# Kernel tuning notes

Hardware: AMD Instinct MI355X
Metric: run time of the kernel (lower is better)

The kernel has to match this reference:

```python
import jax, jax.numpy as jnp
import numpy as np

P, C, D = 65536, 64, 256

def setup_inputs() -> dict:
    key = jax.random.key(0)
    k1, k2, k3, k4 = jax.random.split(key, 4)
    return {
        "protos1": jax.random.normal(k1, (P, D), dtype=jnp.float32),
        "protos2": jax.random.normal(k2, (P, D), dtype=jnp.float32),
        "W": jax.random.normal(k3, (D, D), dtype=jnp.float32) / np.float32(np.sqrt(D)),
        "b": jax.random.normal(k4, (D,), dtype=jnp.float32),
        "num_classes": C,
    }

def _pairwise_dist(x, y):
    # x: (C, n, D), y: (C, m, D) -> squared-euclidean-style dists (C, n, m)
    xs = jnp.sum(x * x, axis=-1)[:, :, None]
    ys = jnp.sum(y * y, axis=-1)[:, None, :]
    return xs + ys - 2.0 * jnp.einsum('cid,cjd->cij', x, y)

def reference(protos1, protos2, W, b, num_classes):
    nc = int(num_classes)
    d = protos1.shape[-1]
    # prototypes[c::num_classes] for all c at once: (P,D) -> (P//C, C, D) -> (C, P//C, D)
    p1 = protos1.reshape(-1, nc, d).transpose(1, 0, 2)
    p2 = protos2.reshape(-1, nc, d).transpose(1, 0, 2)
    # transition: nn.Linear -> x @ W.T + b ; inverse: (x - b) @ inv(W.T)
    p2_inv = (p2 - b) @ jnp.linalg.inv(W.T)
    p1_fwd = p1 @ W.T + b
    a = _pairwise_dist(p1, p2_inv)          # (C, n, n)
    bb = _pairwise_dist(p2, p1_fwd)         # (C, n, n)
    proto_losses_source = jnp.mean(jnp.min(a, axis=2), axis=1)   # (C,)
    proto_losses_target = jnp.mean(jnp.min(bb, axis=2), axis=1)  # (C,)
    return jnp.stack([proto_losses_source, proto_losses_target])  # (2, C)
```

## Files before the change

kernel.cpp:

```cpp
#include <hip/hip_runtime.h>

#define D 256
#define NC 64

using u16 = unsigned short;
using u32 = unsigned int;

typedef __attribute__((ext_vector_type(8))) short bfv8;
typedef __attribute__((ext_vector_type(4))) float f32x4;

__device__ __forceinline__ float bf2f(u32 u) {
  union { u32 i; float f; } v; v.i = u << 16; return v.f;
}
__device__ __forceinline__ u16 f2bf(float f) {
  union { float f; u32 i; } v; v.f = f;
  u32 x = v.i;
  return (u16)((x + 0x7FFFu + ((x >> 16) & 1u)) >> 16);
}
__device__ __forceinline__ u32 pk2(float a, float b) {
  return (u32)f2bf(a) | ((u32)f2bf(b) << 16);
}
__device__ __forceinline__ size_t cmrow(int g) {
  return (size_t)(((g & 63) << 10) | (g >> 6));
}

__device__ __forceinline__ void gload_lds16(const void* src, void* dst) {
  __builtin_amdgcn_global_load_lds(
      (const __attribute__((address_space(1))) void*)src,
      (__attribute__((address_space(3))) void*)dst, 16, 0, 0);
}

#define PH_LDS 70912
#define DIST_LDS 66560

__device__ void gj_body(const float* __restrict__ W, float* __restrict__ IW,
                        char* smem) {
  float (*Ml)[20]    = (float(*)[20])smem;
  float (*Arow)[256] = (float(*)[256])(smem + 20480);
  float (*G)[256]    = (float(*)[256])(smem + 36864);
  u16*  Gfrag        = (u16*)(smem + 53248);
  float (*Pinv)[20]  = (float(*)[20])(smem + 69632);
  const int t = threadIdx.x, w = t >> 6, l = t & 63;
  const int lj = l & 15, lh = l >> 4;
  const int r0 = 16 * w;

  f32x4 x[16];
#pragma unroll
  for (int ct = 0; ct < 16; ++ct)
#pragma unroll
    for (int reg = 0; reg < 4; ++reg)
      x[ct][reg] = W[(size_t)(r0 + 4 * lh + reg) * D + 16 * ct + lj];

  for (int s = 0; s < 16; ++s) {
#pragma unroll
    for (int ct = 0; ct < 16; ++ct)
      if (ct == s)
#pragma unroll
        for (int reg = 0; reg < 4; ++reg)
          Ml[r0 + 4 * lh + reg][lj] = x[ct][reg];
    if (w == s) {
#pragma unroll
      for (int ct = 0; ct < 16; ++ct)
#pragma unroll
        for (int reg = 0; reg < 4; ++reg)
          Arow[4 * lh + reg][16 * ct + lj] = x[ct][reg];
    }
    __syncthreads();
    if (t < 16) {
      float p[16];
      {
        float4 rr0 = *(const float4*)&Ml[16 * s + t][0];
        float4 rr1 = *(const float4*)&Ml[16 * s + t][4];
        float4 rr2 = *(const float4*)&Ml[16 * s + t][8];
        float4 rr3 = *(const float4*)&Ml[16 * s + t][12];
        p[0] = rr0.x; p[1] = rr0.y; p[2] = rr0.z; p[3] = rr0.w;
        p[4] = rr1.x; p[5] = rr1.y; p[6] = rr1.z; p[7] = rr1.w;
        p[8] = rr2.x; p[9] = rr2.y; p[10] = rr2.z; p[11] = rr2.w;
        p[12] = rr3.x; p[13] = rr3.y; p[14] = rr3.z; p[15] = rr3.w;
      }
#pragma unroll
      for (int pp = 0; pp < 16; ++pp) {
        float u[16];
#pragma unroll
        for (int j = 0; j < 16; ++j)
          u[j] = __int_as_float(__builtin_amdgcn_readlane(__float_as_int(p[j]), pp));
        const float pv = u[pp];
        const float d = 1.0f / pv;
        if (t == pp) {
#pragma unroll
          for (int j = 0; j < 16; ++j) p[j] = u[j] * d;
          p[pp] = d;
        } else {
          const float md = p[pp] * d;
          u[pp] = pv + 1.0f;
#pragma unroll
          for (int j = 0; j < 16; ++j) p[j] = fmaf(-md, u[j], p[j]);
        }
      }
#pragma unroll
      for (int j = 0; j < 16; ++j) Pinv[t][j] = p[j];
    }
    __syncthreads();
    {
      const bool inC = ((l >> 2) == s);
      const int co = (l & 3) << 2;
      const int gct = l >> 2;
      const int kk = w;
      float4 g = make_float4(0.f, 0.f, 0.f, 0.f);
#pragma unroll
      for (int q = 0; q < 16; ++q) {
        const float pv = Pinv[kk][q];
        const float4 av = *(const float4*)&Arow[q][4 * l];
        g.x = fmaf(pv, av.x, g.x); g.y = fmaf(pv, av.y, g.y);
        g.z = fmaf(pv, av.z, g.z); g.w = fmaf(pv, av.w, g.w);
      }
      if (inC) {
        g.x = Pinv[kk][co + 0] + (kk == co + 0 ? 1.f : 0.f);
        g.y = Pinv[kk][co + 1] + (kk == co + 1 ? 1.f : 0.f);
        g.z = Pinv[kk][co + 2] + (kk == co + 2 ? 1.f : 0.f);
        g.w = Pinv[kk][co + 3] + (kk == co + 3 ? 1.f : 0.f);
      }
      *(float4*)&G[kk][4 * l] = g;
      const int e0 = kk & 7;
      const int lbase = 16 * (kk >> 3);
      const float gv[4] = {g.x, g.y, g.z, g.w};
#pragma unroll
      for (int cc = 0; cc < 4; ++cc) {
        const int cl = 4 * (l & 3) + cc;
        const u16 hi = f2bf(gv[cc]);
        const u16 lo = f2bf(gv[cc] - bf2f(hi));
        Gfrag[(gct * 64 + lbase + cl) * 8 + e0] = hi;
        Gfrag[(gct * 64 + 32 + lbase + cl) * 8 + e0] = lo;
      }
    }
    __syncthreads();
    bfv8 afr;
    {
      const int row = r0 + lj;
      float4 f0 = *(const float4*)&Ml[row][8 * (lh & 1)];
      float4 f1 = *(const float4*)&Ml[row][8 * (lh & 1) + 4];
      const float fv[8] = {f0.x, f0.y, f0.z, f0.w, f1.x, f1.y, f1.z, f1.w};
      union { bfv8 v; u16 e[8]; } A;
      if (lh < 2) {
#pragma unroll
        for (int e = 0; e < 8; ++e) A.e[e] = f2bf(-fv[e]);
      } else {
#pragma unroll
        for (int e = 0; e < 8; ++e) {
          const float hi = bf2f(f2bf(fv[e]));
          A.e[e] = f2bf(-(fv[e] - hi));
        }
      }
      afr = A.v;
    }
    if (w != s) {
#pragma unroll
      for (int ct = 0; ct < 16; ++ct) {
        bfv8 b1 = *(const bfv8*)&Gfrag[(ct * 64 + l) * 8];
        bfv8 b2 = *(const bfv8*)&Gfrag[(ct * 64 + (l ^ 32)) * 8];
        x[ct] = __builtin_amdgcn_mfma_f32_16x16x32_bf16(afr, b1, x[ct], 0, 0, 0);
        x[ct] = __builtin_amdgcn_mfma_f32_16x16x32_bf16(afr, b2, x[ct], 0, 0, 0);
      }
    } else {
#pragma unroll
      for (int ct = 0; ct < 16; ++ct) {
        if (ct == s) {
#pragma unroll
          for (int reg = 0; reg < 4; ++reg)
            x[ct][reg] = Pinv[4 * lh + reg][lj];
        } else {
#pragma unroll
          for (int reg = 0; reg < 4; ++reg)
            x[ct][reg] = G[4 * lh + reg][16 * ct + lj];
        }
      }
    }
    __syncthreads();
  }
#pragma unroll
  for (int ct = 0; ct < 16; ++ct)
#pragma unroll
    for (int reg = 0; reg < 4; ++reg)
      IW[(size_t)(r0 + 4 * lh + reg) * D + 16 * ct + lj] = x[ct][reg];
}

template <int MODE, bool WRITE_NRM>
__device__ void prep_body(const float* __restrict__ Ain,
                          const u16* __restrict__ Brows,
                          const float* __restrict__ biasv,
                          u16* __restrict__ Out, float* __restrict__ nrm,
                          float* __restrict__ nfp, int it, char* smem) {
  const int tx = threadIdx.x, ww = tx >> 6, l = tx & 63;
  const int mw = ww >> 3, nw = ww & 7, l4 = l >> 4, lm = l & 15;
  char* Ab = smem;
  float* nfpart = (float*)(smem + 65536);

  bfv8 bfr[2][8];
#pragma unroll
  for (int nf2 = 0; nf2 < 2; ++nf2)
#pragma unroll
    for (int ks = 0; ks < 8; ++ks)
      bfr[nf2][ks] = *(const bfv8*)(Brows +
          (size_t)(nw * 32 + nf2 * 16 + lm) * D + ks * 32 + l4 * 8);

  {
    const int r = tx >> 3, sg = tx & 7;
    const float* arow = Ain + (size_t)(it * 128 + r) * D + sg * 32;
    float ss = 0.f;
#pragma unroll
    for (int g2 = 0; g2 < 4; ++g2) {
      float4 v0 = *(const float4*)(arow + g2 * 8);
      float4 v1 = *(const float4*)(arow + g2 * 8 + 4);
      ss = fmaf(v0.x, v0.x, fmaf(v0.y, v0.y, fmaf(v0.z, v0.z, fmaf(v0.w, v0.w, ss))));
      ss = fmaf(v1.x, v1.x, fmaf(v1.y, v1.y, fmaf(v1.z, v1.z, fmaf(v1.w, v1.w, ss))));
      uint4 w4;
      w4.x = pk2(v0.x, v0.y); w4.y = pk2(v0.z, v0.w);
      w4.z = pk2(v1.x, v1.y); w4.w = pk2(v1.z, v1.w);
      *(uint4*)(Ab + (sg * 8 + (r >> 4)) * 1024 + ((r & 15) + g2 * 16) * 16) = w4;
    }
    ss += __shfl_xor(ss, 1, 64);
    ss += __shfl_xor(ss, 2, 64);
    ss += __shfl_xor(ss, 4, 64);
    if (WRITE_NRM && sg == 0) nrm[cmrow(it * 128 + r)] = ss;
  }
  __syncthreads();

  const bfv8* A8 = (const bfv8*)Ab;
  f32x4 acc[4][2];
#pragma unroll
  for (int mf = 0; mf < 4; ++mf) {
    acc[mf][0] = f32x4{0.f, 0.f, 0.f, 0.f};
    acc[mf][1] = f32x4{0.f, 0.f, 0.f, 0.f};
  }
#pragma unroll
  for (int ks = 0; ks < 8; ++ks)
#pragma unroll
    for (int mf = 0; mf < 4; ++mf) {
      bfv8 a = A8[(ks * 8 + mw * 4 + mf) * 64 + l];
      acc[mf][0] = __builtin_amdgcn_mfma_f32_16x16x32_bf16(a, bfr[0][ks], acc[mf][0], 0, 0, 0);
      acc[mf][1] = __builtin_amdgcn_mfma_f32_16x16x32_bf16(a, bfr[1][ks], acc[mf][1], 0, 0, 0);
    }

  float bias[2];
  if (MODE == 0) {
#pragma unroll
    for (int nf2 = 0; nf2 < 2; ++nf2)
      bias[nf2] = biasv[nw * 32 + nf2 * 16 + lm];
  } else {
#pragma unroll
    for (int nf2 = 0; nf2 < 2; ++nf2) {
      float pd = 0.f;
#pragma unroll
      for (int ks = 0; ks < 8; ++ks) {
        float4 b0 = *(const float4*)(biasv + ks * 32 + l4 * 8);
        float4 b1 = *(const float4*)(biasv + ks * 32 + l4 * 8 + 4);
        pd = fmaf(b0.x, bf2f((u16)bfr[nf2][ks][0]), pd);
        pd = fmaf(b0.y, bf2f((u16)bfr[nf2][ks][1]), pd);
        pd = fmaf(b0.z, bf2f((u16)bfr[nf2][ks][2]), pd);
        pd = fmaf(b0.w, bf2f((u16)bfr[nf2][ks][3]), pd);
        pd = fmaf(b1.x, bf2f((u16)bfr[nf2][ks][4]), pd);
        pd = fmaf(b1.y, bf2f((u16)bfr[nf2][ks][5]), pd);
        pd = fmaf(b1.z, bf2f((u16)bfr[nf2][ks][6]), pd);
        pd = fmaf(b1.w, bf2f((u16)bfr[nf2][ks][7]), pd);
      }
      pd += __shfl_xor(pd, 16, 64);
      pd += __shfl_xor(pd, 32, 64);
      bias[nf2] = -pd;
    }
  }

#pragma unroll
  for (int mf = 0; mf < 4; ++mf)
#pragma unroll
    for (int rr = 0; rr < 4; ++rr) {
      const int g = it * 128 + mw * 64 + mf * 16 + l4 * 4 + rr;
      const size_t orow = cmrow(g) * D;
      float v2 = 0.f;
#pragma unroll
      for (int nf2 = 0; nf2 < 2; ++nf2) {
        const float v = acc[mf][nf2][rr] + bias[nf2];
        const u16 hv = f2bf(v);
        Out[orow + nw * 32 + nf2 * 16 + lm] = hv;
        const float vr = bf2f(hv);
        v2 = fmaf(vr, vr, v2);
      }
      v2 += __shfl_xor(v2, 1, 64);
      v2 += __shfl_xor(v2, 2, 64);
      v2 += __shfl_xor(v2, 4, 64);
      v2 += __shfl_xor(v2, 8, 64);
      if (lm == 0) nfpart[nw * 128 + mw * 64 + mf * 16 + l4 * 4 + rr] = v2;
    }
  __syncthreads();
  if (tx < 128) {
    float s = 0.f;
#pragma unroll
    for (int q = 0; q < 8; ++q) s += nfpart[q * 128 + tx];
    nfp[cmrow(it * 128 + tx)] = s;
  }
}

__device__ void norms_role(const float* __restrict__ p2, float* __restrict__ n2,
                           int idx) {
  const int tx = threadIdx.x, q = tx & 3;
#pragma unroll
  for (int rep = 0; rep < 8; ++rep) {
    const int g = idx * 2048 + rep * 256 + (tx >> 2);
    const float* row = p2 + (size_t)g * D + q * 64;
    float ss = 0.f;
#pragma unroll
    for (int g2 = 0; g2 < 16; ++g2) {
      float4 v = *(const float4*)(row + g2 * 4);
      ss = fmaf(v.x, v.x, fmaf(v.y, v.y, fmaf(v.z, v.z, fmaf(v.w, v.w, ss))));
    }
    ss += __shfl_xor(ss, 1, 64);
    ss += __shfl_xor(ss, 2, 64);
    if (q == 0) n2[cmrow(g)] = ss;
  }
}

__global__ __launch_bounds__(1024, 1) void phase1_kernel(
    const float* __restrict__ p1, const float* __restrict__ p2,
    const float* __restrict__ W, const u16* __restrict__ Wb,
    const float* __restrict__ bv, u16* __restrict__ Fb,
    float* __restrict__ n1, float* __restrict__ n2,
    float* __restrict__ nf, float* __restrict__ IWa) {
  extern __shared__ char smem[];
  const int b = blockIdx.x;
  if (b == 0) {
    gj_body(W, IWa, smem);
  } else if (b <= 512) {
    prep_body<0, true>(p1, Wb, bv, Fb, n1, nf, b - 1, smem);
  } else {
    norms_role(p2, n2, b - 513);
  }
}

__global__ __launch_bounds__(1024, 1) void phase3_kernel(
    const float* __restrict__ p2, const u16* __restrict__ IWb,
    const float* __restrict__ bv, u16* __restrict__ Qb,
    float* __restrict__ nq) {
  extern __shared__ char smem[];
  prep_body<1, false>(p2, IWb, bv, Qb, nullptr, nq, blockIdx.x, smem);
}

__global__ __launch_bounds__(256) void nr_residual(const float* __restrict__ W,
                                                   const float* __restrict__ X,
                                                   float* __restrict__ R) {
  __shared__ float wrow[D];
  const int i = blockIdx.x, j = threadIdx.x;
  wrow[j] = W[i * D + j];
  __syncthreads();
  float acc = 0.f;
#pragma unroll 8
  for (int k = 0; k < D; ++k) acc = fmaf(wrow[k], X[k * D + j], acc);
  R[i * D + j] = (i == j ? 2.0f : 0.0f) - acc;
}

__global__ __launch_bounds__(256) void nr_mult_bf16(const float* __restrict__ X,
                                                    const float* __restrict__ R,
                                                    u16* __restrict__ Yb) {
  __shared__ float xrow[D];
  const int i = blockIdx.x, j = threadIdx.x;
  xrow[j] = X[i * D + j];
  __syncthreads();
  float acc = 0.f;
#pragma unroll 8
  for (int k = 0; k < D; ++k) acc = fmaf(xrow[k], R[k * D + j], acc);
  Yb[i * D + j] = f2bf(acc);
}

__global__ __launch_bounds__(256) void wconv(const float* __restrict__ W,
                                             u16* __restrict__ Wb) {
  const int i = blockIdx.x * 256 + threadIdx.x;
  Wb[i] = f2bf(W[i]);
}

__global__ __launch_bounds__(256, 2) void dist_kernel(
    const float* __restrict__ p1, const float* __restrict__ p2,
    const u16* __restrict__ Qb, const u16* __restrict__ Fb,
    const float* __restrict__ n1, const float* __restrict__ n2,
    const float* __restrict__ nq, const float* __restrict__ nf,
    float* __restrict__ partial) {
  extern __shared__ char smem[];
  const int bid = blockIdx.x;
  const int lb = (bid & 7) * 128 + (bid >> 3);
  const int c = lb >> 4, dir = (lb >> 3) & 1, it = lb & 7;
  const float* Ain = dir ? p2 : p1;
  const u16* Bin = dir ? Fb : Qb;
  const float* nA = dir ? n2 : n1;
  const float* nB = dir ? nf : nq;
  const int tx = threadIdx.x, wid = tx >> 6, l = tx & 63;
  const int l4 = l >> 4, lm = l & 15;

  auto issue_b = [&](int half, int jt) {
    const size_t base = ((size_t)(c << 10) + jt * 128) * D;
#pragma unroll
    for (int jf = 0; jf < 8; ++jf) {
      const u16* src = Bin + base + (size_t)(jf * 16 + lm) * D
                       + half * 128 + wid * 32 + l4 * 8;
      gload_lds16(src, smem + half * 32768 + (wid * 8 + jf) * 1024);
    }
  };

  issue_b(0, 0);
  bfv8 afr[2][8];
  const float* abase = Ain + ((size_t)(it * 128 + wid * 32) * NC + c) * D;
#pragma unroll
  for (int m = 0; m < 2; ++m)
#pragma unroll
    for (int ks = 0; ks < 8; ++ks) {
      const float* ap = abase + (size_t)(m * 16 + lm) * (NC * D) + ks * 32 + l4 * 8;
      float4 v0 = *(const float4*)(ap);
      float4 v1 = *(const float4*)(ap + 4);
      union { bfv8 v; uint4 u; } cv;
      cv.u.x = pk2(v0.x, v0.y); cv.u.y = pk2(v0.z, v0.w);
      cv.u.z = pk2(v1.x, v1.y); cv.u.w = pk2(v1.z, v1.w);
      afr[m][ks] = cv.v;
    }
  float na[2][4];
#pragma unroll
  for (int m = 0; m < 2; ++m)
#pragma unroll
    for (int rr = 0; rr < 4; ++rr)
      na[m][rr] = nA[(c << 10) + it * 128 + wid * 32 + m * 16 + l4 * 4 + rr];
  float minv[2][4];
#pragma unroll
  for (int m = 0; m < 2; ++m)
#pragma unroll
    for (int rr = 0; rr < 4; ++rr) minv[m][rr] = 3.0e38f;
  __syncthreads();

  const bfv8* lds8 = (const bfv8*)smem;
  for (int jt = 0; jt < 8; ++jt) {
    f32x4 acc[2][8];
#pragma unroll
    for (int m = 0; m < 2; ++m)
#pragma unroll
      for (int n = 0; n < 8; ++n) acc[m][n] = f32x4{0.f, 0.f, 0.f, 0.f};
    float nbv[8];
#pragma unroll
    for (int n = 0; n < 8; ++n)
      nbv[n] = nB[(c << 10) + jt * 128 + n * 16 + lm];
    issue_b(1, jt);
#pragma unroll
    for (int ks = 0; ks < 4; ++ks) {
      bfv8 bb[8];
#pragma unroll
      for (int n = 0; n < 8; ++n) bb[n] = lds8[(ks * 8 + n) * 64 + l];
#pragma unroll
      for (int m = 0; m < 2; ++m)
#pragma unroll
        for (int n = 0; n < 8; ++n)
          acc[m][n] = __builtin_amdgcn_mfma_f32_16x16x32_bf16(afr[m][ks], bb[n], acc[m][n], 0, 0, 0);
    }
    __syncthreads();
    if (jt < 7) issue_b(0, jt + 1);
#pragma unroll
    for (int ks = 4; ks < 8; ++ks) {
      bfv8 bb[8];
#pragma unroll
      for (int n = 0; n < 8; ++n) bb[n] = lds8[2048 + ((ks - 4) * 8 + n) * 64 + l];
#pragma unroll
      for (int m = 0; m < 2; ++m)
#pragma unroll
        for (int n = 0; n < 8; ++n)
          acc[m][n] = __builtin_amdgcn_mfma_f32_16x16x32_bf16(afr[m][ks], bb[n], acc[m][n], 0, 0, 0);
    }
#pragma unroll
    for (int m = 0; m < 2; ++m)
#pragma unroll
      for (int n = 0; n < 8; ++n)
#pragma unroll
        for (int rr = 0; rr < 4; ++rr) {
          const float dd = na[m][rr] + nbv[n] - 2.0f * acc[m][n][rr];
          minv[m][rr] = fminf(minv[m][rr], dd);
        }
    __syncthreads();
  }
  float* red = (float*)(smem + 65536);
#pragma unroll
  for (int m = 0; m < 2; ++m)
#pragma unroll
    for (int rr = 0; rr < 4; ++rr) {
      float mm = minv[m][rr];
      mm = fminf(mm, __shfl_xor(mm, 1, 64));
      mm = fminf(mm, __shfl_xor(mm, 2, 64));
      mm = fminf(mm, __shfl_xor(mm, 4, 64));
      mm = fminf(mm, __shfl_xor(mm, 8, 64));
      if (lm == 0) red[wid * 32 + m * 16 + l4 * 4 + rr] = mm;
    }
  __syncthreads();
  if (tx < 128) {
    float v = red[tx];
#pragma unroll
    for (int off = 32; off; off >>= 1) v += __shfl_xor(v, off, 64);
    if ((tx & 63) == 0) red[128 + (tx >> 6)] = v;
  }
  __syncthreads();
  if (tx == 0) partial[lb] = red[128] + red[129];
}

__global__ void finalize_kernel(const float* __restrict__ partial,
                                float* __restrict__ out) {
  const int tx = threadIdx.x;
  if (tx >= 128) return;
  const int dir = tx >> 6, c = tx & 63;
  float s = 0.f;
#pragma unroll
  for (int it = 0; it < 8; ++it) s += partial[(c << 4) | (dir << 3) | it];
  out[dir * 64 + c] = s * (1.0f / 1024.0f);
}

extern "C" void kernel_launch(void* const* d_in, const int* in_sizes, int n_in,
                              void* d_out, int out_size, void* d_ws, size_t ws_size,
                              hipStream_t stream) {
  const float* p1 = (const float*)d_in[0];
  const float* p2 = (const float*)d_in[1];
  const float* W  = (const float*)d_in[2];
  const float* bv = (const float*)d_in[3];
  float* out = (float*)d_out;
  char* ws = (char*)d_ws;
  float* n1   = (float*)(ws);
  float* n2   = (float*)(ws + (256 << 10));
  float* nf   = (float*)(ws + (512 << 10));
  float* nq   = (float*)(ws + (768 << 10));
  float* partial = (float*)(ws + (1024 << 10));
  u16* Wb  = (u16*)(ws + (1032 << 10));
  u16* IWb = (u16*)(ws + (1160 << 10));
  float* IWa = (float*)(ws + (1288 << 10));
  float* Rt  = (float*)(ws + (1544 << 10));
  u16* Fb  = (u16*)(ws + (2048 << 10));
  u16* Qb  = (u16*)(ws + (2048 << 10) + (32u << 20));

  hipFuncSetAttribute((const void*)phase1_kernel,
                      hipFuncAttributeMaxDynamicSharedMemorySize, PH_LDS);
  hipFuncSetAttribute((const void*)phase3_kernel,
                      hipFuncAttributeMaxDynamicSharedMemorySize, PH_LDS);
  hipFuncSetAttribute((const void*)dist_kernel,
                      hipFuncAttributeMaxDynamicSharedMemorySize, DIST_LDS);

  wconv<<<256, 256, 0, stream>>>(W, Wb);
  phase1_kernel<<<545, 1024, PH_LDS, stream>>>(p1, p2, W, Wb, bv, Fb,
                                               n1, n2, nf, IWa);
  nr_residual<<<256, 256, 0, stream>>>(W, IWa, Rt);
  nr_mult_bf16<<<256, 256, 0, stream>>>(IWa, Rt, IWb);
  phase3_kernel<<<512, 1024, PH_LDS, stream>>>(p2, IWb, bv, Qb, nq);
  dist_kernel<<<1024, 256, DIST_LDS, stream>>>(p1, p2, Qb, Fb, n1, n2,
                                               nq, nf, partial);
  finalize_kernel<<<1, 128, 0, stream>>>(partial, out);
}
```

Measured before the change: 298.1 us.

## Overlap target-direction distance pass with NR residual and trim Gauss-Jordan syncs

Splits the distance kernel into two directions. The target direction, which needs only the forward projection, now runs alongside the Newton-Schulz residual in a combined kernel before the inverse path finishes. The source direction runs after phase3. Separately, the Gauss-Jordan inverse now has every wave invert the 16x16 pivot block redundantly and broadcast it via readlane, removing one block barrier per step and one at the end of each step. This adds redundant ALU work per wave and a heterogeneous launch with mismatched block roles.

```diff
diff --git a/kernel.cpp b/kernel.cpp
--- a/kernel.cpp
+++ b/kernel.cpp
@@ -35,11 +35,11 @@
 
 __device__ void gj_body(const float* __restrict__ W, float* __restrict__ IW,
                         char* smem) {
-  float (*Ml)[20]    = (float(*)[20])smem;
-  float (*Arow)[256] = (float(*)[256])(smem + 20480);
-  float (*G)[256]    = (float(*)[256])(smem + 36864);
-  u16*  Gfrag        = (u16*)(smem + 53248);
-  float (*Pinv)[20]  = (float(*)[20])(smem + 69632);
+  float (*Arow)[260]   = (float(*)[260])smem;
+  float (*G)[256]      = (float(*)[256])(smem + 16640);
+  u16*  Gfrag          = (u16*)(smem + 33024);
+  float (*Ml)[16][20]  = (float(*)[16][20])(smem + 49408);
+  float (*PinvL)[16]   = (float(*)[16])(smem + 69888);
   const int t = threadIdx.x, w = t >> 6, l = t & 63;
   const int lj = l & 15, lh = l >> 4;
   const int r0 = 16 * w;
@@ -57,7 +57,7 @@
       if (ct == s)
 #pragma unroll
         for (int reg = 0; reg < 4; ++reg)
-          Ml[r0 + 4 * lh + reg][lj] = x[ct][reg];
+          Ml[w][4 * lh + reg][lj] = x[ct][reg];
     if (w == s) {
 #pragma unroll
       for (int ct = 0; ct < 16; ++ct)
@@ -66,18 +66,19 @@
           Arow[4 * lh + reg][16 * ct + lj] = x[ct][reg];
     }
     __syncthreads();
-    if (t < 16) {
-      float p[16];
-      {
-        float4 rr0 = *(const float4*)&Ml[16 * s + t][0];
-        float4 rr1 = *(const float4*)&Ml[16 * s + t][4];
-        float4 rr2 = *(const float4*)&Ml[16 * s + t][8];
-        float4 rr3 = *(const float4*)&Ml[16 * s + t][12];
-        p[0] = rr0.x; p[1] = rr0.y; p[2] = rr0.z; p[3] = rr0.w;
-        p[4] = rr1.x; p[5] = rr1.y; p[6] = rr1.z; p[7] = rr1.w;
-        p[8] = rr2.x; p[9] = rr2.y; p[10] = rr2.z; p[11] = rr2.w;
-        p[12] = rr3.x; p[13] = rr3.y; p[14] = rr3.z; p[15] = rr3.w;
-      }
+    float p[16];
+#pragma unroll
+    for (int j = 0; j < 16; ++j) p[j] = 0.f;
+    if (l < 16) {
+      const float* ar = &Arow[l][16 * s];
+      float4 rr0 = *(const float4*)(ar);
+      float4 rr1 = *(const float4*)(ar + 4);
+      float4 rr2 = *(const float4*)(ar + 8);
+      float4 rr3 = *(const float4*)(ar + 12);
+      p[0] = rr0.x; p[1] = rr0.y; p[2] = rr0.z; p[3] = rr0.w;
+      p[4] = rr1.x; p[5] = rr1.y; p[6] = rr1.z; p[7] = rr1.w;
+      p[8] = rr2.x; p[9] = rr2.y; p[10] = rr2.z; p[11] = rr2.w;
+      p[12] = rr3.x; p[13] = rr3.y; p[14] = rr3.z; p[15] = rr3.w;
 #pragma unroll
       for (int pp = 0; pp < 16; ++pp) {
         float u[16];
@@ -86,7 +87,7 @@
           u[j] = __int_as_float(__builtin_amdgcn_readlane(__float_as_int(p[j]), pp));
         const float pv = u[pp];
         const float d = 1.0f / pv;
-        if (t == pp) {
+        if (l == pp) {
 #pragma unroll
           for (int j = 0; j < 16; ++j) p[j] = u[j] * d;
           p[pp] = d;
@@ -97,32 +98,35 @@
           for (int j = 0; j < 16; ++j) p[j] = fmaf(-md, u[j], p[j]);
         }
       }
-#pragma unroll
-      for (int j = 0; j < 16; ++j) Pinv[t][j] = p[j];
-    }
-    __syncthreads();
+      if (w == s) {
+#pragma unroll
+        for (int j = 0; j < 16; ++j) PinvL[l][j] = p[j];
+      }
+    }
+    float pw[16];
+#pragma unroll
+    for (int q = 0; q < 16; ++q)
+      pw[q] = __int_as_float(__builtin_amdgcn_readlane(__float_as_int(p[q]), w));
     {
       const bool inC = ((l >> 2) == s);
       const int co = (l & 3) << 2;
+      float4 g = make_float4(0.f, 0.f, 0.f, 0.f);
+#pragma unroll
+      for (int q = 0; q < 16; ++q) {
+        const float4 av = *(const float4*)&Arow[q][4 * l];
+        g.x = fmaf(pw[q], av.x, g.x); g.y = fmaf(pw[q], av.y, g.y);
+        g.z = fmaf(pw[q], av.z, g.z); g.w = fmaf(pw[q], av.w, g.w);
+      }
+      if (inC) {
+        g.x = pw[co + 0] + (w == co + 0 ? 1.f : 0.f);
+        g.y = pw[co + 1] + (w == co + 1 ? 1.f : 0.f);
+        g.z = pw[co + 2] + (w == co + 2 ? 1.f : 0.f);
+        g.w = pw[co + 3] + (w == co + 3 ? 1.f : 0.f);
+      }
+      *(float4*)&G[w][4 * l] = g;
+      const int e0 = w & 7;
+      const int lbase = 16 * (w >> 3);
       const int gct = l >> 2;
-      const int kk = w;
-      float4 g = make_float4(0.f, 0.f, 0.f, 0.f);
-#pragma unroll
-      for (int q = 0; q < 16; ++q) {
-        const float pv = Pinv[kk][q];
-        const float4 av = *(const float4*)&Arow[q][4 * l];
-        g.x = fmaf(pv, av.x, g.x); g.y = fmaf(pv, av.y, g.y);
-        g.z = fmaf(pv, av.z, g.z); g.w = fmaf(pv, av.w, g.w);
-      }
-      if (inC) {
-        g.x = Pinv[kk][co + 0] + (kk == co + 0 ? 1.f : 0.f);
-        g.y = Pinv[kk][co + 1] + (kk == co + 1 ? 1.f : 0.f);
-        g.z = Pinv[kk][co + 2] + (kk == co + 2 ? 1.f : 0.f);
-        g.w = Pinv[kk][co + 3] + (kk == co + 3 ? 1.f : 0.f);
-      }
-      *(float4*)&G[kk][4 * l] = g;
-      const int e0 = kk & 7;
-      const int lbase = 16 * (kk >> 3);
       const float gv[4] = {g.x, g.y, g.z, g.w};
 #pragma unroll
       for (int cc = 0; cc < 4; ++cc) {
@@ -136,9 +140,8 @@
     __syncthreads();
     bfv8 afr;
     {
-      const int row = r0 + lj;
-      float4 f0 = *(const float4*)&Ml[row][8 * (lh & 1)];
-      float4 f1 = *(const float4*)&Ml[row][8 * (lh & 1) + 4];
+      float4 f0 = *(const float4*)&Ml[w][lj][8 * (lh & 1)];
+      float4 f1 = *(const float4*)&Ml[w][lj][8 * (lh & 1) + 4];
       const float fv[8] = {f0.x, f0.y, f0.z, f0.w, f1.x, f1.y, f1.z, f1.w};
       union { bfv8 v; u16 e[8]; } A;
       if (lh < 2) {
@@ -167,7 +170,7 @@
         if (ct == s) {
 #pragma unroll
           for (int reg = 0; reg < 4; ++reg)
-            x[ct][reg] = Pinv[4 * lh + reg][lj];
+            x[ct][reg] = PinvL[4 * lh + reg][lj];
         } else {
 #pragma unroll
           for (int reg = 0; reg < 4; ++reg)
@@ -175,8 +178,8 @@
         }
       }
     }
-    __syncthreads();
-  }
+  }
+  __syncthreads();
 #pragma unroll
   for (int ct = 0; ct < 16; ++ct)
 #pragma unroll
@@ -343,19 +346,6 @@
   prep_body<1, false>(p2, IWb, bv, Qb, nullptr, nq, blockIdx.x, smem);
 }
 
-__global__ __launch_bounds__(256) void nr_residual(const float* __restrict__ W,
-                                                   const float* __restrict__ X,
-                                                   float* __restrict__ R) {
-  __shared__ float wrow[D];
-  const int i = blockIdx.x, j = threadIdx.x;
-  wrow[j] = W[i * D + j];
-  __syncthreads();
-  float acc = 0.f;
-#pragma unroll 8
-  for (int k = 0; k < D; ++k) acc = fmaf(wrow[k], X[k * D + j], acc);
-  R[i * D + j] = (i == j ? 2.0f : 0.0f) - acc;
-}
-
 __global__ __launch_bounds__(256) void nr_mult_bf16(const float* __restrict__ X,
                                                     const float* __restrict__ R,
                                                     u16* __restrict__ Yb) {
@@ -375,20 +365,14 @@
   Wb[i] = f2bf(W[i]);
 }
 
-__global__ __launch_bounds__(256, 2) void dist_kernel(
-    const float* __restrict__ p1, const float* __restrict__ p2,
-    const u16* __restrict__ Qb, const u16* __restrict__ Fb,
-    const float* __restrict__ n1, const float* __restrict__ n2,
-    const float* __restrict__ nq, const float* __restrict__ nf,
-    float* __restrict__ partial) {
-  extern __shared__ char smem[];
-  const int bid = blockIdx.x;
-  const int lb = (bid & 7) * 128 + (bid >> 3);
-  const int c = lb >> 4, dir = (lb >> 3) & 1, it = lb & 7;
-  const float* Ain = dir ? p2 : p1;
-  const u16* Bin = dir ? Fb : Qb;
-  const float* nA = dir ? n2 : n1;
-  const float* nB = dir ? nf : nq;
+template <int DIR>
+__device__ void dist_body(const float* __restrict__ Ain,
+                          const u16* __restrict__ Bin,
+                          const float* __restrict__ nA,
+                          const float* __restrict__ nB,
+                          float* __restrict__ partial, int bid, char* smem) {
+  const int lb = (bid & 7) * 64 + (bid >> 3);
+  const int c = lb >> 3, it = lb & 7;
   const int tx = threadIdx.x, wid = tx >> 6, l = tx & 63;
   const int l4 = l >> 4, lm = l & 15;
 
@@ -497,7 +481,36 @@
     if ((tx & 63) == 0) red[128 + (tx >> 6)] = v;
   }
   __syncthreads();
-  if (tx == 0) partial[lb] = red[128] + red[129];
+  if (tx == 0) partial[(c << 4) | (DIR << 3) | it] = red[128] + red[129];
+}
+
+__global__ __launch_bounds__(256, 2) void phase2_kernel(
+    const float* __restrict__ p2, const u16* __restrict__ Fb,
+    const float* __restrict__ n2, const float* __restrict__ nf,
+    const float* __restrict__ W, const float* __restrict__ IWa,
+    float* __restrict__ Rt, float* __restrict__ partial) {
+  extern __shared__ char smem[];
+  const int b = blockIdx.x;
+  if (b < 512) {
+    dist_body<1>(p2, Fb, n2, nf, partial, b, smem);
+  } else {
+    float* wrow = (float*)smem;
+    const int i = b - 512, j = threadIdx.x;
+    wrow[j] = W[i * D + j];
+    __syncthreads();
+    float acc = 0.f;
+#pragma unroll 8
+    for (int k = 0; k < D; ++k) acc = fmaf(wrow[k], IWa[k * D + j], acc);
+    Rt[i * D + j] = (i == j ? 2.0f : 0.0f) - acc;
+  }
+}
+
+__global__ __launch_bounds__(256, 2) void dist0_kernel(
+    const float* __restrict__ p1, const u16* __restrict__ Qb,
+    const float* __restrict__ n1, const float* __restrict__ nq,
+    float* __restrict__ partial) {
+  extern __shared__ char smem[];
+  dist_body<0>(p1, Qb, n1, nq, partial, blockIdx.x, smem);
 }
 
 __global__ void finalize_kernel(const float* __restrict__ partial,
@@ -534,18 +547,20 @@
 
   hipFuncSetAttribute((const void*)phase1_kernel,
                       hipFuncAttributeMaxDynamicSharedMemorySize, PH_LDS);
+  hipFuncSetAttribute((const void*)phase2_kernel,
+                      hipFuncAttributeMaxDynamicSharedMemorySize, DIST_LDS);
   hipFuncSetAttribute((const void*)phase3_kernel,
                       hipFuncAttributeMaxDynamicSharedMemorySize, PH_LDS);
-  hipFuncSetAttribute((const void*)dist_kernel,
+  hipFuncSetAttribute((const void*)dist0_kernel,
                       hipFuncAttributeMaxDynamicSharedMemorySize, DIST_LDS);
 
   wconv<<<256, 256, 0, stream>>>(W, Wb);
   phase1_kernel<<<545, 1024, PH_LDS, stream>>>(p1, p2, W, Wb, bv, Fb,
                                                n1, n2, nf, IWa);
-  nr_residual<<<256, 256, 0, stream>>>(W, IWa, Rt);
+  phase2_kernel<<<768, 256, DIST_LDS, stream>>>(p2, Fb, n2, nf, W, IWa,
+                                                Rt, partial);
   nr_mult_bf16<<<256, 256, 0, stream>>>(IWa, Rt, IWb);
   phase3_kernel<<<512, 1024, PH_LDS, stream>>>(p2, IWb, bv, Qb, nq);
-  dist_kernel<<<1024, 256, DIST_LDS, stream>>>(p1, p2, Qb, Fb, n1, n2,
-                                               nq, nf, partial);
+  dist0_kernel<<<512, 256, DIST_LDS, stream>>>(p1, Qb, n1, nq, partial);
   finalize_kernel<<<1, 128, 0, stream>>>(partial, out);
 }
```

Result: slower. 346.7 us (+16.3%).

## Overlap target-direction distance pass with Newton residual; tune Gauss-Jordan LDS use

Applied to the files above, without the earlier changes.

The distance kernel is split by direction. The dir=1 pass (p2 vs forward-projected p1) only needs phase1 outputs, so it now runs in a combined phase2 launch alongside the Newton-Raphson residual blocks, overlapping with the inverse-refinement chain. The dir=0 pass runs after phase3. Inside the Gauss-Jordan body, the A-fragment conversion moves before the barrier, Gfrag gets padded strides to avoid LDS bank conflicts, and the second B fragment comes from a permlane32 swap instead of a second LDS read. Costs are a larger LDS allocation and more code paths.

```diff
diff --git a/kernel.cpp b/kernel.cpp
--- a/kernel.cpp
+++ b/kernel.cpp
@@ -8,6 +8,7 @@
 
 typedef __attribute__((ext_vector_type(8))) short bfv8;
 typedef __attribute__((ext_vector_type(4))) float f32x4;
+typedef __attribute__((ext_vector_type(2))) int v2i;
 
 __device__ __forceinline__ float bf2f(u32 u) {
   union { u32 i; float f; } v; v.i = u << 16; return v.f;
@@ -30,7 +31,7 @@
       (__attribute__((address_space(3))) void*)dst, 16, 0, 0);
 }
 
-#define PH_LDS 70912
+#define PH_LDS 71168
 #define DIST_LDS 66560
 
 __device__ void gj_body(const float* __restrict__ W, float* __restrict__ IW,
@@ -39,10 +40,11 @@
   float (*Arow)[256] = (float(*)[256])(smem + 20480);
   float (*G)[256]    = (float(*)[256])(smem + 36864);
   u16*  Gfrag        = (u16*)(smem + 53248);
-  float (*Pinv)[20]  = (float(*)[20])(smem + 69632);
+  float (*Pinv)[20]  = (float(*)[20])(smem + 69888);
   const int t = threadIdx.x, w = t >> 6, l = t & 63;
   const int lj = l & 15, lh = l >> 4;
   const int r0 = 16 * w;
+  const bool lo32 = (l < 32);
 
   f32x4 x[16];
 #pragma unroll
@@ -64,6 +66,25 @@
 #pragma unroll
         for (int reg = 0; reg < 4; ++reg)
           Arow[4 * lh + reg][16 * ct + lj] = x[ct][reg];
+    }
+    bfv8 afr;
+    {
+      const int row = r0 + lj;
+      float4 f0 = *(const float4*)&Ml[row][8 * (lh & 1)];
+      float4 f1 = *(const float4*)&Ml[row][8 * (lh & 1) + 4];
+      const float fv[8] = {f0.x, f0.y, f0.z, f0.w, f1.x, f1.y, f1.z, f1.w};
+      union { bfv8 v; u16 e[8]; } A;
+      if (lh < 2) {
+#pragma unroll
+        for (int e = 0; e < 8; ++e) A.e[e] = f2bf(-fv[e]);
+      } else {
+#pragma unroll
+        for (int e = 0; e < 8; ++e) {
+          const float hi = bf2f(f2bf(fv[e]));
+          A.e[e] = f2bf(-(fv[e] - hi));
+        }
+      }
+      afr = A.v;
     }
     __syncthreads();
     if (t < 16) {
@@ -129,37 +150,33 @@
         const int cl = 4 * (l & 3) + cc;
         const u16 hi = f2bf(gv[cc]);
         const u16 lo = f2bf(gv[cc] - bf2f(hi));
-        Gfrag[(gct * 64 + lbase + cl) * 8 + e0] = hi;
-        Gfrag[(gct * 64 + 32 + lbase + cl) * 8 + e0] = lo;
-      }
-    }
-    __syncthreads();
-    bfv8 afr;
-    {
-      const int row = r0 + lj;
-      float4 f0 = *(const float4*)&Ml[row][8 * (lh & 1)];
-      float4 f1 = *(const float4*)&Ml[row][8 * (lh & 1) + 4];
-      const float fv[8] = {f0.x, f0.y, f0.z, f0.w, f1.x, f1.y, f1.z, f1.w};
-      union { bfv8 v; u16 e[8]; } A;
-      if (lh < 2) {
-#pragma unroll
-        for (int e = 0; e < 8; ++e) A.e[e] = f2bf(-fv[e]);
-      } else {
-#pragma unroll
-        for (int e = 0; e < 8; ++e) {
-          const float hi = bf2f(f2bf(fv[e]));
-          A.e[e] = f2bf(-(fv[e] - hi));
+        Gfrag[gct * 520 + (lbase + cl) * 8 + e0] = hi;
+        Gfrag[gct * 520 + (32 + lbase + cl) * 8 + e0] = lo;
+      }
+    }
+    __syncthreads();
+    if (w != s) {
+#pragma unroll
+      for (int ct = 0; ct < 16; ++ct) {
+        union { bfv8 v; uint4 u; } B1, B2;
+        B1.v = *(const bfv8*)&Gfrag[ct * 520 + l * 8];
+#if __has_builtin(__builtin_amdgcn_permlane32_swap)
+        {
+          v2i r;
+          r = __builtin_amdgcn_permlane32_swap((int)B1.u.x, (int)B1.u.x, false, false);
+          B2.u.x = lo32 ? (u32)r.y : (u32)r.x;
+          r = __builtin_amdgcn_permlane32_swap((int)B1.u.y, (int)B1.u.y, false, false);
+          B2.u.y = lo32 ? (u32)r.y : (u32)r.x;
+          r = __builtin_amdgcn_permlane32_swap((int)B1.u.z, (int)B1.u.z, false, false);
+          B2.u.z = lo32 ? (u32)r.y : (u32)r.x;
+          r = __builtin_amdgcn_permlane32_swap((int)B1.u.w, (int)B1.u.w, false, false);
+          B2.u.w = lo32 ? (u32)r.y : (u32)r.x;
         }
-      }
-      afr = A.v;
-    }
-    if (w != s) {
-#pragma unroll
-      for (int ct = 0; ct < 16; ++ct) {
-        bfv8 b1 = *(const bfv8*)&Gfrag[(ct * 64 + l) * 8];
-        bfv8 b2 = *(const bfv8*)&Gfrag[(ct * 64 + (l ^ 32)) * 8];
-        x[ct] = __builtin_amdgcn_mfma_f32_16x16x32_bf16(afr, b1, x[ct], 0, 0, 0);
-        x[ct] = __builtin_amdgcn_mfma_f32_16x16x32_bf16(afr, b2, x[ct], 0, 0, 0);
+#else
+        B2.v = *(const bfv8*)&Gfrag[ct * 520 + (l ^ 32) * 8];
+#endif
+        x[ct] = __builtin_amdgcn_mfma_f32_16x16x32_bf16(afr, B1.v, x[ct], 0, 0, 0);
+        x[ct] = __builtin_amdgcn_mfma_f32_16x16x32_bf16(afr, B2.v, x[ct], 0, 0, 0);
       }
     } else {
 #pragma unroll
@@ -343,19 +360,6 @@
   prep_body<1, false>(p2, IWb, bv, Qb, nullptr, nq, blockIdx.x, smem);
 }
 
-__global__ __launch_bounds__(256) void nr_residual(const float* __restrict__ W,
-                                                   const float* __restrict__ X,
-                                                   float* __restrict__ R) {
-  __shared__ float wrow[D];
-  const int i = blockIdx.x, j = threadIdx.x;
-  wrow[j] = W[i * D + j];
-  __syncthreads();
-  float acc = 0.f;
-#pragma unroll 8
-  for (int k = 0; k < D; ++k) acc = fmaf(wrow[k], X[k * D + j], acc);
-  R[i * D + j] = (i == j ? 2.0f : 0.0f) - acc;
-}
-
 __global__ __launch_bounds__(256) void nr_mult_bf16(const float* __restrict__ X,
                                                     const float* __restrict__ R,
                                                     u16* __restrict__ Yb) {
@@ -375,20 +379,14 @@
   Wb[i] = f2bf(W[i]);
 }
 
-__global__ __launch_bounds__(256, 2) void dist_kernel(
-    const float* __restrict__ p1, const float* __restrict__ p2,
-    const u16* __restrict__ Qb, const u16* __restrict__ Fb,
-    const float* __restrict__ n1, const float* __restrict__ n2,
-    const float* __restrict__ nq, const float* __restrict__ nf,
-    float* __restrict__ partial) {
-  extern __shared__ char smem[];
-  const int bid = blockIdx.x;
-  const int lb = (bid & 7) * 128 + (bid >> 3);
-  const int c = lb >> 4, dir = (lb >> 3) & 1, it = lb & 7;
-  const float* Ain = dir ? p2 : p1;
-  const u16* Bin = dir ? Fb : Qb;
-  const float* nA = dir ? n2 : n1;
-  const float* nB = dir ? nf : nq;
+template <int DIR>
+__device__ void dist_body(const float* __restrict__ Ain,
+                          const u16* __restrict__ Bin,
+                          const float* __restrict__ nA,
+                          const float* __restrict__ nB,
+                          float* __restrict__ partial, int bid, char* smem) {
+  const int lb = (bid & 7) * 64 + (bid >> 3);
+  const int c = lb >> 3, it = lb & 7;
   const int tx = threadIdx.x, wid = tx >> 6, l = tx & 63;
   const int l4 = l >> 4, lm = l & 15;
 
@@ -497,7 +495,36 @@
     if ((tx & 63) == 0) red[128 + (tx >> 6)] = v;
   }
   __syncthreads();
-  if (tx == 0) partial[lb] = red[128] + red[129];
+  if (tx == 0) partial[(c << 4) | (DIR << 3) | it] = red[128] + red[129];
+}
+
+__global__ __launch_bounds__(256, 2) void phase2_kernel(
+    const float* __restrict__ p2, const u16* __restrict__ Fb,
+    const float* __restrict__ n2, const float* __restrict__ nf,
+    const float* __restrict__ W, const float* __restrict__ IWa,
+    float* __restrict__ Rt, float* __restrict__ partial) {
+  extern __shared__ char smem[];
+  const int b = blockIdx.x;
+  if (b < 512) {
+    dist_body<1>(p2, Fb, n2, nf, partial, b, smem);
+  } else {
+    float* wrow = (float*)smem;
+    const int i = b - 512, j = threadIdx.x;
+    wrow[j] = W[i * D + j];
+    __syncthreads();
+    float acc = 0.f;
+#pragma unroll 8
+    for (int k = 0; k < D; ++k) acc = fmaf(wrow[k], IWa[k * D + j], acc);
+    Rt[i * D + j] = (i == j ? 2.0f : 0.0f) - acc;
+  }
+}
+
+__global__ __launch_bounds__(256, 2) void dist0_kernel(
+    const float* __restrict__ p1, const u16* __restrict__ Qb,
+    const float* __restrict__ n1, const float* __restrict__ nq,
+    float* __restrict__ partial) {
+  extern __shared__ char smem[];
+  dist_body<0>(p1, Qb, n1, nq, partial, blockIdx.x, smem);
 }
 
 __global__ void finalize_kernel(const float* __restrict__ partial,
@@ -534,18 +561,20 @@
 
   hipFuncSetAttribute((const void*)phase1_kernel,
                       hipFuncAttributeMaxDynamicSharedMemorySize, PH_LDS);
+  hipFuncSetAttribute((const void*)phase2_kernel,
+                      hipFuncAttributeMaxDynamicSharedMemorySize, DIST_LDS);
   hipFuncSetAttribute((const void*)phase3_kernel,
                       hipFuncAttributeMaxDynamicSharedMemorySize, PH_LDS);
-  hipFuncSetAttribute((const void*)dist_kernel,
+  hipFuncSetAttribute((const void*)dist0_kernel,
                       hipFuncAttributeMaxDynamicSharedMemorySize, DIST_LDS);
 
   wconv<<<256, 256, 0, stream>>>(W, Wb);
   phase1_kernel<<<545, 1024, PH_LDS, stream>>>(p1, p2, W, Wb, bv, Fb,
                                                n1, n2, nf, IWa);
-  nr_residual<<<256, 256, 0, stream>>>(W, IWa, Rt);
+  phase2_kernel<<<768, 256, DIST_LDS, stream>>>(p2, Fb, n2, nf, W, IWa,
+                                                Rt, partial);
   nr_mult_bf16<<<256, 256, 0, stream>>>(IWa, Rt, IWb);
   phase3_kernel<<<512, 1024, PH_LDS, stream>>>(p2, IWb, bv, Qb, nq);
-  dist_kernel<<<1024, 256, DIST_LDS, stream>>>(p1, p2, Qb, Fb, n1, n2,
-                                               nq, nf, partial);
+  dist0_kernel<<<512, 256, DIST_LDS, stream>>>(p1, Qb, n1, nq, partial);
   finalize_kernel<<<1, 128, 0, stream>>>(partial, out);
 }
```

Result: no change. 297.6 us (-0.2%).
